# Performance work log

Hardware: AMD Instinct MI355X
Metric: run time of the kernel (lower is better)

The kernel has to match this reference:

```python
import jax, jax.numpy as jnp
import numpy as np

F = 1024      # features
CF = 768      # context_features
H = 8         # num_heads
D = 64        # head_features
MID = H * D   # 512
SCALE = D ** -0.5


def _ln(x, g, b):
    m = jnp.mean(x, axis=-1, keepdims=True)
    v = jnp.var(x, axis=-1, keepdims=True)
    return (x - m) / jnp.sqrt(v + 1e-5) * g + b


def _attention(x, ctx, ng, nb, ncg, ncb, wq, wkv, wo, bo):
    # pre-norms (Attention.forward)
    xn = _ln(x, ng, nb)
    cn = _ln(ctx, ncg, ncb)
    q = xn @ wq                              # [b, n, MID]
    k, v = jnp.split(cn @ wkv, 2, axis=-1)   # [b, m, MID] each
    b, n, _ = q.shape
    m = k.shape[1]
    q = q.reshape(b, n, H, D).transpose(0, 2, 1, 3)  # b h n d
    k = k.reshape(b, m, H, D).transpose(0, 2, 1, 3)
    v = v.reshape(b, m, H, D).transpose(0, 2, 1, 3)
    sim = jnp.einsum('bhnd,bhmd->bhnm', q, k) * SCALE   # use_rel_pos=False
    attn = jax.nn.softmax(sim, axis=-1)
    out = jnp.einsum('bhnm,bhmd->bhnd', attn, v)
    out = out.transpose(0, 2, 1, 3).reshape(b, n, MID)
    return out @ wo + bo


def setup_inputs() -> dict:
    key = jax.random.key(0)
    ks = jax.random.split(key, 16)
    s = 0.02
    inp = {
        'x': jax.random.normal(ks[0], (4, 2048, F), jnp.float32),
        'context': jax.random.normal(ks[1], (4, 512, CF), jnp.float32),
        # self-attention params
        'sa_ng': jnp.ones((F,), jnp.float32),
        'sa_nb': jnp.zeros((F,), jnp.float32),
        'sa_ncg': jnp.ones((F,), jnp.float32),
        'sa_ncb': jnp.zeros((F,), jnp.float32),
        'sa_wq': jax.random.normal(ks[2], (F, MID), jnp.float32) * s,
        'sa_wkv': jax.random.normal(ks[3], (F, 2 * MID), jnp.float32) * s,
        'sa_wo': jax.random.normal(ks[4], (MID, F), jnp.float32) * s,
        'sa_bo': jnp.zeros((F,), jnp.float32),
        # cross-attention params
        'ca_ng': jnp.ones((F,), jnp.float32),
        'ca_nb': jnp.zeros((F,), jnp.float32),
        'ca_ncg': jnp.ones((CF,), jnp.float32),
        'ca_ncb': jnp.zeros((CF,), jnp.float32),
        'ca_wq': jax.random.normal(ks[5], (F, MID), jnp.float32) * s,
        'ca_wkv': jax.random.normal(ks[6], (CF, 2 * MID), jnp.float32) * s,
        'ca_wo': jax.random.normal(ks[7], (MID, F), jnp.float32) * s,
        'ca_bo': jnp.zeros((F,), jnp.float32),
    }
    return inp


def reference(x, context,
              sa_ng, sa_nb, sa_ncg, sa_ncb, sa_wq, sa_wkv, sa_wo, sa_bo,
              ca_ng, ca_nb, ca_ncg, ca_ncb, ca_wq, ca_wkv, ca_wo, ca_bo):
    # AttentionBlock.forward: x = self_attn(x) + x; x = cross_attn(x, ctx) + x
    x = _attention(x, x, sa_ng, sa_nb, sa_ncg, sa_ncb, sa_wq, sa_wkv, sa_wo, sa_bo) + x
    x = _attention(x, context, ca_ng, ca_nb, ca_ncg, ca_ncb, ca_wq, ca_wkv, ca_wo, ca_bo) + x
    return x
```

## Files before the change

### kernel.cpp

```cpp
#include <hip/hip_runtime.h>
#include <hip/hip_bf16.h>

typedef __bf16 bf16x8 __attribute__((ext_vector_type(8)));
typedef float  f32x4  __attribute__((ext_vector_type(4)));

#define MFMA16(a, b, c) __builtin_amdgcn_mfma_f32_16x16x32_bf16((a), (b), (c), 0, 0, 0)

__device__ __forceinline__ float fast_exp2(float x) {
#if __has_builtin(__builtin_amdgcn_exp2f)
    return __builtin_amdgcn_exp2f(x);
#else
    return exp2f(x);
#endif
}

__device__ __forceinline__ void async16(void* lds, const void* g) {
    __builtin_amdgcn_global_load_lds(
        (const __attribute__((address_space(1))) unsigned int*)g,
        (__attribute__((address_space(3))) unsigned int*)lds, 16, 0, 0);
}

__device__ __forceinline__ void tconv_tile(const float* __restrict__ W,
                                           __bf16* __restrict__ WT,
                                           int K, int N, int id, int nbx,
                                           __bf16 (*t)[65]) {
    int n0 = (id % nbx) * 64, k0 = (id / nbx) * 64;
    int tx = threadIdx.x & 63, ty = threadIdx.x >> 6;
#pragma unroll
    for (int r = ty; r < 64; r += 4)
        t[r][tx] = (__bf16)W[(size_t)(k0 + r) * N + n0 + tx];
    __syncthreads();
#pragma unroll
    for (int rr = ty; rr < 64; rr += 4)
        WT[(size_t)(n0 + rr) * K + k0 + tx] = t[tx][rr];
}

__global__ __launch_bounds__(256) void tconv6_kernel(
    const float* W0, __bf16* T0, const float* W1, __bf16* T1,
    const float* W2, __bf16* T2, const float* W3, __bf16* T3,
    const float* W4, __bf16* T4, const float* W5, __bf16* T5) {
    __shared__ __bf16 t[64][65];
    int id = blockIdx.x;
    if (id < 128)      tconv_tile(W0, T0, 1024, 512,  id,       8,  t);
    else if (id < 384) tconv_tile(W1, T1, 1024, 1024, id - 128, 16, t);
    else if (id < 512) tconv_tile(W2, T2, 512,  1024, id - 384, 16, t);
    else if (id < 640) tconv_tile(W3, T3, 1024, 512,  id - 512, 8,  t);
    else if (id < 832) tconv_tile(W4, T4, 768,  1024, id - 640, 16, t);
    else               tconv_tile(W5, T5, 512,  1024, id - 832, 16, t);
}

template <int C>
__device__ __forceinline__ void ln_body(const float* __restrict__ xr,
                                        const float* __restrict__ g,
                                        const float* __restrict__ b,
                                        __bf16* __restrict__ orow,
                                        float* p1, float* p2) {
    constexpr int NP = (C == 1024) ? 4 : 3;
    float v[NP], s1 = 0.f, s2 = 0.f;
    if constexpr (C == 1024) {
        float4 f = *(const float4*)&xr[threadIdx.x * 4];
        v[0] = f.x; v[1] = f.y; v[2] = f.z; v[3] = f.w;
#pragma unroll
        for (int i = 0; i < 4; i++) { s1 += v[i]; s2 += v[i] * v[i]; }
    } else {
#pragma unroll
        for (int i = 0; i < 3; i++) {
            v[i] = xr[threadIdx.x + i * 256];
            s1 += v[i]; s2 += v[i] * v[i];
        }
    }
#pragma unroll
    for (int off = 1; off < 64; off <<= 1) {
        s1 += __shfl_xor(s1, off);
        s2 += __shfl_xor(s2, off);
    }
    int wave = threadIdx.x >> 6;
    if ((threadIdx.x & 63) == 0) { p1[wave] = s1; p2[wave] = s2; }
    __syncthreads();
    s1 = p1[0] + p1[1] + p1[2] + p1[3];
    s2 = p2[0] + p2[1] + p2[2] + p2[3];
    float mean = s1 / C;
    float rstd = rsqrtf(s2 / C - mean * mean + 1e-5f);
    if constexpr (C == 1024) {
        union { __bf16 h[4]; unsigned long long u; } pk;
#pragma unroll
        for (int i = 0; i < 4; i++) {
            int c = threadIdx.x * 4 + i;
            pk.h[i] = (__bf16)((v[i] - mean) * rstd * g[c] + b[c]);
        }
        *(unsigned long long*)&orow[threadIdx.x * 4] = pk.u;
    } else {
#pragma unroll
        for (int i = 0; i < 3; i++) {
            int c = threadIdx.x + i * 256;
            orow[c] = (__bf16)((v[i] - mean) * rstd * g[c] + b[c]);
        }
    }
}

__global__ __launch_bounds__(256) void ln2_kernel(const float* __restrict__ x,
                                                  const float* __restrict__ g1,
                                                  const float* __restrict__ b1,
                                                  const float* __restrict__ g2,
                                                  const float* __restrict__ b2,
                                                  __bf16* __restrict__ o1,
                                                  __bf16* __restrict__ o2) {
    constexpr int C = 1024;
    int row = blockIdx.x;
    const float* xr = x + (size_t)row * C;
    float4 f = *(const float4*)&xr[threadIdx.x * 4];
    float v[4] = {f.x, f.y, f.z, f.w};
    float s1 = 0.f, s2 = 0.f;
#pragma unroll
    for (int i = 0; i < 4; i++) { s1 += v[i]; s2 += v[i] * v[i]; }
#pragma unroll
    for (int off = 1; off < 64; off <<= 1) {
        s1 += __shfl_xor(s1, off);
        s2 += __shfl_xor(s2, off);
    }
    __shared__ float p1[4], p2[4];
    int wave = threadIdx.x >> 6;
    if ((threadIdx.x & 63) == 0) { p1[wave] = s1; p2[wave] = s2; }
    __syncthreads();
    s1 = p1[0] + p1[1] + p1[2] + p1[3];
    s2 = p2[0] + p2[1] + p2[2] + p2[3];
    float mean = s1 / C;
    float rstd = rsqrtf(s2 / C - mean * mean + 1e-5f);
    union { __bf16 h[4]; unsigned long long u; } pk1, pk2;
#pragma unroll
    for (int i = 0; i < 4; i++) {
        int c = threadIdx.x * 4 + i;
        float nv = (v[i] - mean) * rstd;
        pk1.h[i] = (__bf16)(nv * g1[c] + b1[c]);
        pk2.h[i] = (__bf16)(nv * g2[c] + b2[c]);
    }
    *(unsigned long long*)&o1[(size_t)row * C + threadIdx.x * 4] = pk1.u;
    *(unsigned long long*)&o2[(size_t)row * C + threadIdx.x * 4] = pk2.u;
}

__global__ __launch_bounds__(256) void ln_cross_kernel(
    const float* __restrict__ x1, const float* __restrict__ g1, const float* __restrict__ b1,
    __bf16* __restrict__ o1,
    const float* __restrict__ ctx, const float* __restrict__ g2, const float* __restrict__ b2,
    __bf16* __restrict__ o2, int rows1) {
    __shared__ float p1[4], p2[4];
    int id = blockIdx.x;
    if (id < rows1) {
        ln_body<1024>(x1 + (size_t)id * 1024, g1, b1, o1 + (size_t)id * 1024, p1, p2);
    } else {
        int row = id - rows1;
        ln_body<768>(ctx + (size_t)row * 768, g2, b2, o2 + (size_t)row * 768, p1, p2);
    }
}

template <int EPI>
__device__ __forceinline__ void gemm_core(const __bf16* __restrict__ A,
                                          const __bf16* __restrict__ BT,
                                          void* __restrict__ Cout,
                                          int N, int K, int bm, int bn,
                                          const float* __restrict__ bias,
                                          const float* __restrict__ res,
                                          float scale,
                                          __bf16* Al, __bf16* Bl) {
    int tid = threadIdx.x;
    int lane = tid & 63, wave = tid >> 6;
    int quad = lane >> 4, l15 = lane & 15;
    int wm = wave >> 1, wn = wave & 1;
    const __bf16* Ab = A + (size_t)(bm * 128) * K;
    const __bf16* Bb = BT + (size_t)(bn * 128) * K;
    f32x4 acc[4][4] = {};
    for (int k0 = 0; k0 < K; k0 += 64) {
#pragma unroll
        for (int j = 0; j < 4; j++) {
            int sbase = wave * 256 + j * 64;
            int s = sbase + lane;
            int r = s >> 3, c = (s & 7) ^ (r & 7);
            async16((char*)Al + sbase * 16, &Ab[(size_t)r * K + k0 + c * 8]);
            async16((char*)Bl + sbase * 16, &Bb[(size_t)r * K + k0 + c * 8]);
        }
        __syncthreads();
#pragma unroll
        for (int ks = 0; ks < 2; ks++) {
            bf16x8 a[4], b[4];
#pragma unroll
            for (int i = 0; i < 4; i++) {
                int row = wm * 64 + i * 16 + l15;
                a[i] = *(const bf16x8*)&Al[row * 64 + ((ks * 4 + quad) ^ (row & 7)) * 8];
            }
#pragma unroll
            for (int t = 0; t < 4; t++) {
                int row = wn * 64 + t * 16 + l15;
                b[t] = *(const bf16x8*)&Bl[row * 64 + ((ks * 4 + quad) ^ (row & 7)) * 8];
            }
#pragma unroll
            for (int i = 0; i < 4; i++)
#pragma unroll
                for (int t = 0; t < 4; t++) acc[i][t] = MFMA16(a[i], b[t], acc[i][t]);
        }
        __syncthreads();
    }
#pragma unroll
    for (int i = 0; i < 4; i++) {
#pragma unroll
        for (int t = 0; t < 4; t++) {
#pragma unroll
            for (int r = 0; r < 4; r++) {
                int row = bm * 128 + wm * 64 + i * 16 + quad * 4 + r;
                int col = bn * 128 + wn * 64 + t * 16 + l15;
                float vv = acc[i][t][r];
                if (EPI == 0) {
                    ((__bf16*)Cout)[(size_t)row * N + col] = (__bf16)(vv * scale);
                } else {
                    ((float*)Cout)[(size_t)row * N + col] =
                        vv + bias[col] + res[(size_t)row * N + col];
                }
            }
        }
    }
}

template <int EPI>
__global__ __launch_bounds__(256) void gemm_bt(const __bf16* __restrict__ A,
                                               const __bf16* __restrict__ BT,
                                               void* __restrict__ Cout,
                                               int M, int N, int K,
                                               const float* __restrict__ bias,
                                               const float* __restrict__ res) {
    __shared__ __align__(16) __bf16 Al[128 * 64];
    __shared__ __align__(16) __bf16 Bl[128 * 64];
    gemm_core<EPI>(A, BT, Cout, N, K, blockIdx.x, blockIdx.y, bias, res, 1.0f, Al, Bl);
}

__global__ __launch_bounds__(256) void gemm_fused3(
    const __bf16* A0, const __bf16* B0, __bf16* C0, int N0, int K0, int nbn0, float sc0,
    const __bf16* A1, const __bf16* B1, __bf16* C1, int N1, int K1, int nbn1, float sc1,
    const __bf16* A2, const __bf16* B2, __bf16* C2, int N2, int K2, int nbn2, float sc2,
    int c0, int c1) {
    __shared__ __align__(16) __bf16 Al[128 * 64];
    __shared__ __align__(16) __bf16 Bl[128 * 64];
    int id = blockIdx.x;
    if (id < c0) {
        gemm_core<0>(A0, B0, C0, N0, K0, id / nbn0, id % nbn0, nullptr, nullptr, sc0, Al, Bl);
    } else if (id < c1) {
        id -= c0;
        gemm_core<0>(A1, B1, C1, N1, K1, id / nbn1, id % nbn1, nullptr, nullptr, sc1, Al, Bl);
    } else {
        id -= c1;
        gemm_core<0>(A2, B2, C2, N2, K2, id / nbn2, id % nbn2, nullptr, nullptr, sc2, Al, Bl);
    }
}

__global__ __launch_bounds__(256) void flash_kernel(const __bf16* __restrict__ q,
                                                    const __bf16* __restrict__ kb,
                                                    const __bf16* __restrict__ vt,
                                                    __bf16* __restrict__ out,
                                                    int n, int m) {
    __shared__ __align__(16) __bf16 Qs[64 * 64];
    __shared__ __align__(16) __bf16 Ks[64 * 64];
    __shared__ __align__(16) __bf16 VTs[64 * 64];
    __shared__ __align__(16) __bf16 Ps[64 * 64];
    int tid = threadIdx.x;
    int lane = tid & 63, w = tid >> 6;
    int quad = lane >> 4, l15 = lane & 15;
    int qt = blockIdx.x, h = blockIdx.y, b = blockIdx.z;
    const size_t BM = (size_t)gridDim.z * m;
    const int qrow = w * 16 + l15;

#pragma unroll
    for (int j = 0; j < 2; j++) {
        int sbase = w * 128 + j * 64;
        int s = sbase + lane;
        int r = s >> 3, c = (s & 7) ^ (r & 7);
        async16((char*)Qs + sbase * 16,
                &q[(size_t)(b * n + qt * 64 + r) * 512 + h * 64 + c * 8]);
    }

    f32x4 acc[4] = {};
    float l_part = 0.f;

    int nkt = m / 64;
    for (int kt = 0; kt < nkt; kt++) {
#pragma unroll
        for (int j = 0; j < 2; j++) {
            int sbase = w * 128 + j * 64;
            int s = sbase + lane;
            int r = s >> 3, c = (s & 7) ^ (r & 7);
            async16((char*)Ks + sbase * 16,
                    &kb[(size_t)(b * m + kt * 64 + r) * 512 + h * 64 + c * 8]);
            async16((char*)VTs + sbase * 16,
                    &vt[(size_t)(h * 64 + r) * BM + b * m + kt * 64 + c * 8]);
        }
        __syncthreads();

        f32x4 sacc[4] = {};
#pragma unroll
        for (int kk = 0; kk < 64; kk += 32) {
            int jb = ((kk >> 3) + quad) ^ (qrow & 7);
            bf16x8 bq = *(const bf16x8*)&Qs[qrow * 64 + jb * 8];
#pragma unroll
            for (int t = 0; t < 4; t++) {
                int krow = t * 16 + l15;
                int ja = ((kk >> 3) + quad) ^ (krow & 7);
                bf16x8 ak = *(const bf16x8*)&Ks[krow * 64 + ja * 8];
                sacc[t] = MFMA16(ak, bq, sacc[t]);
            }
        }

#pragma unroll
        for (int t = 0; t < 4; t++) {
            float e0 = fast_exp2(sacc[t][0]);
            float e1 = fast_exp2(sacc[t][1]);
            float e2 = fast_exp2(sacc[t][2]);
            float e3 = fast_exp2(sacc[t][3]);
            l_part += (e0 + e1) + (e2 + e3);
            union { __bf16 h[4]; unsigned long long u; } pk;
            pk.h[0] = (__bf16)e0; pk.h[1] = (__bf16)e1;
            pk.h[2] = (__bf16)e2; pk.h[3] = (__bf16)e3;
            int chunk = t * 2 + (quad >> 1);
            int off = qrow * 64 + (chunk ^ (qrow & 7)) * 8 + (quad & 1) * 4;
            *(unsigned long long*)&Ps[off] = pk.u;
        }

#pragma unroll
        for (int kk = 0; kk < 64; kk += 32) {
            int jp = ((kk >> 3) + quad) ^ (qrow & 7);
            bf16x8 ap = *(const bf16x8*)&Ps[qrow * 64 + jp * 8];
#pragma unroll
            for (int t2 = 0; t2 < 4; t2++) {
                int drow = t2 * 16 + l15;
                int jv = ((kk >> 3) + quad) ^ (drow & 7);
                bf16x8 bv = *(const bf16x8*)&VTs[drow * 64 + jv * 8];
                acc[t2] = MFMA16(ap, bv, acc[t2]);
            }
        }
        __syncthreads();
    }

    l_part += __shfl_xor(l_part, 16);
    l_part += __shfl_xor(l_part, 32);
    float rinv = 1.0f / l_part;
#pragma unroll
    for (int r = 0; r < 4; r++) {
        float rl = __shfl(rinv, quad * 4 + r);
        int row = b * n + qt * 64 + w * 16 + quad * 4 + r;
#pragma unroll
        for (int t2 = 0; t2 < 4; t2++)
            out[(size_t)row * 512 + h * 64 + t2 * 16 + l15] =
                (__bf16)(acc[t2][r] * rl);
    }
}

extern "C" void kernel_launch(void* const* d_in, const int* in_sizes, int n_in,
                              void* d_out, int out_size, void* d_ws, size_t ws_size,
                              hipStream_t stream) {
    const float* x      = (const float*)d_in[0];
    const float* ctx    = (const float*)d_in[1];
    const float* sa_ng  = (const float*)d_in[2];
    const float* sa_nb  = (const float*)d_in[3];
    const float* sa_ncg = (const float*)d_in[4];
    const float* sa_ncb = (const float*)d_in[5];
    const float* sa_wq  = (const float*)d_in[6];
    const float* sa_wkv = (const float*)d_in[7];
    const float* sa_wo  = (const float*)d_in[8];
    const float* sa_bo  = (const float*)d_in[9];
    const float* ca_ng  = (const float*)d_in[10];
    const float* ca_nb  = (const float*)d_in[11];
    const float* ca_ncg = (const float*)d_in[12];
    const float* ca_ncb = (const float*)d_in[13];
    const float* ca_wq  = (const float*)d_in[14];
    const float* ca_wkv = (const float*)d_in[15];
    const float* ca_wo  = (const float*)d_in[16];
    const float* ca_bo  = (const float*)d_in[17];
    float* out = (float*)d_out;

    const int B = 4, N = 2048, M = 512, F = 1024, CF = 768, MID = 512;
    const int ROWS = B * N;
    const int CROWS = B * M;
    const float QSCALE = 0.125f * 1.4426950408889634f;

    char* ws = (char*)d_ws;
    size_t off = 0;
    auto alloc = [&](size_t bytes) {
        void* p = ws + off;
        off = (off + bytes + 255) & ~(size_t)255;
        return p;
    };
    __bf16* wqT   = (__bf16*)alloc((size_t)MID * F * 2);
    __bf16* wkvT  = (__bf16*)alloc((size_t)(2 * MID) * F * 2);
    __bf16* woT   = (__bf16*)alloc((size_t)F * MID * 2);
    __bf16* cwqT  = (__bf16*)alloc((size_t)MID * F * 2);
    __bf16* cwkvT = (__bf16*)alloc((size_t)(2 * MID) * CF * 2);
    __bf16* cwoT  = (__bf16*)alloc((size_t)F * MID * 2);
    __bf16* xn1   = (__bf16*)alloc((size_t)ROWS * F * 2);
    __bf16* xn2   = (__bf16*)alloc((size_t)ROWS * F * 2);
    __bf16* qb    = (__bf16*)alloc((size_t)ROWS * MID * 2);
    __bf16* kb    = (__bf16*)alloc((size_t)ROWS * MID * 2);
    __bf16* vt    = (__bf16*)alloc((size_t)MID * ROWS * 2);
    __bf16* ao    = (__bf16*)alloc((size_t)ROWS * MID * 2);
    float*  x1    = (float*)alloc((size_t)ROWS * F * 4);
    (void)ws_size; (void)in_sizes; (void)n_in; (void)out_size;

    dim3 blk(256);

    tconv6_kernel<<<dim3(960), blk, 0, stream>>>(
        sa_wq, wqT, sa_wkv, wkvT, sa_wo, woT, ca_wq, cwqT, ca_wkv, cwkvT, ca_wo, cwoT);

    ln2_kernel<<<dim3(ROWS), blk, 0, stream>>>(x, sa_ng, sa_nb, sa_ncg, sa_ncb, xn1, xn2);
    {
        int c0 = (ROWS / 128) * (MID / 128);
        int c1 = c0 + (ROWS / 128) * (MID / 128);
        int c2 = c1 + (MID / 128) * (ROWS / 128);
        gemm_fused3<<<dim3(c2), blk, 0, stream>>>(
            xn1, wqT, qb, MID, F, MID / 128, QSCALE,
            xn2, wkvT, kb, MID, F, MID / 128, 1.0f,
            wkvT + (size_t)MID * F, xn2, vt, ROWS, F, ROWS / 128, 1.0f,
            c0, c1);
    }
    flash_kernel<<<dim3(N / 64, 8, B), blk, 0, stream>>>(qb, kb, vt, ao, N, N);
    gemm_bt<1><<<dim3(ROWS / 128, F / 128), blk, 0, stream>>>(
        ao, woT, x1, ROWS, F, MID, sa_bo, x);

    ln_cross_kernel<<<dim3(ROWS + CROWS), blk, 0, stream>>>(
        x1, ca_ng, ca_nb, xn1, ctx, ca_ncg, ca_ncb, xn2, ROWS);
    {
        int c0 = (ROWS / 128) * (MID / 128);
        int c1 = c0 + (CROWS / 128) * (MID / 128);
        int c2 = c1 + (MID / 128) * (CROWS / 128);
        gemm_fused3<<<dim3(c2), blk, 0, stream>>>(
            xn1, cwqT, qb, MID, F, MID / 128, QSCALE,
            xn2, cwkvT, kb, MID, CF, MID / 128, 1.0f,
            cwkvT + (size_t)MID * CF, xn2, vt, CROWS, CF, CROWS / 128, 1.0f,
            c0, c1);
    }
    flash_kernel<<<dim3(N / 64, 8, B), blk, 0, stream>>>(qb, kb, vt, ao, N, M);
    gemm_bt<1><<<dim3(ROWS / 128, F / 128), blk, 0, stream>>>(
        ao, cwoT, out, ROWS, F, MID, ca_bo, x1);
}
```

Baseline: 325.8 us.

## Double-buffer K/V tiles in flash kernel and keep Q in registers

```diff
diff --git a/kernel.cpp b/kernel.cpp
--- a/kernel.cpp
+++ b/kernel.cpp
@@ -255,9 +255,8 @@
                                                     const __bf16* __restrict__ vt,
                                                     __bf16* __restrict__ out,
                                                     int n, int m) {
-    __shared__ __align__(16) __bf16 Qs[64 * 64];
-    __shared__ __align__(16) __bf16 Ks[64 * 64];
-    __shared__ __align__(16) __bf16 VTs[64 * 64];
+    __shared__ __align__(16) __bf16 Ks[2][64 * 64];
+    __shared__ __align__(16) __bf16 VTs[2][64 * 64];
     __shared__ __align__(16) __bf16 Ps[64 * 64];
     int tid = threadIdx.x;
     int lane = tid & 63, w = tid >> 6;
@@ -266,42 +265,53 @@
     const size_t BM = (size_t)gridDim.z * m;
     const int qrow = w * 16 + l15;
 
-#pragma unroll
-    for (int j = 0; j < 2; j++) {
-        int sbase = w * 128 + j * 64;
-        int s = sbase + lane;
-        int r = s >> 3, c = (s & 7) ^ (r & 7);
-        async16((char*)Qs + sbase * 16,
-                &q[(size_t)(b * n + qt * 64 + r) * 512 + h * 64 + c * 8]);
-    }
+    const __bf16* qrp = &q[(size_t)(b * n + qt * 64 + qrow) * 512 + h * 64];
+    bf16x8 bq0 = *(const bf16x8*)&qrp[quad * 8];
+    bf16x8 bq1 = *(const bf16x8*)&qrp[(4 + quad) * 8];
+
+    int s0 = w * 128 + lane, s1 = s0 + 64;
+    int r0 = s0 >> 3, c0 = (s0 & 7) ^ (r0 & 7);
+    int r1 = s1 >> 3, c1 = (s1 & 7) ^ (r1 & 7);
+    const int sb0 = (w * 128) * 16, sb1 = sb0 + 64 * 16;
+    const __bf16* ksrc0 = &kb[(size_t)(b * m + r0) * 512 + h * 64 + (size_t)c0 * 8];
+    const __bf16* ksrc1 = &kb[(size_t)(b * m + r1) * 512 + h * 64 + (size_t)c1 * 8];
+    const __bf16* vsrc0 = &vt[(size_t)(h * 64 + r0) * BM + b * m + (size_t)c0 * 8];
+    const __bf16* vsrc1 = &vt[(size_t)(h * 64 + r1) * BM + b * m + (size_t)c1 * 8];
+    const size_t kadv = (size_t)64 * 512;
+    const int vadv = 64;
 
     f32x4 acc[4] = {};
     float l_part = 0.f;
-
     int nkt = m / 64;
+
+    async16((char*)Ks[0] + sb0, ksrc0);
+    async16((char*)Ks[0] + sb1, ksrc1);
+    async16((char*)VTs[0] + sb0, vsrc0);
+    async16((char*)VTs[0] + sb1, vsrc1);
+
     for (int kt = 0; kt < nkt; kt++) {
-#pragma unroll
-        for (int j = 0; j < 2; j++) {
-            int sbase = w * 128 + j * 64;
-            int s = sbase + lane;
-            int r = s >> 3, c = (s & 7) ^ (r & 7);
-            async16((char*)Ks + sbase * 16,
-                    &kb[(size_t)(b * m + kt * 64 + r) * 512 + h * 64 + c * 8]);
-            async16((char*)VTs + sbase * 16,
-                    &vt[(size_t)(h * 64 + r) * BM + b * m + kt * 64 + c * 8]);
-        }
+        const __bf16* Kc = Ks[kt & 1];
+        const __bf16* Vc = VTs[kt & 1];
         __syncthreads();
+        if (kt + 1 < nkt) {
+            __bf16* Kn = Ks[(kt + 1) & 1];
+            __bf16* Vn = VTs[(kt + 1) & 1];
+            ksrc0 += kadv; ksrc1 += kadv; vsrc0 += vadv; vsrc1 += vadv;
+            async16((char*)Kn + sb0, ksrc0);
+            async16((char*)Kn + sb1, ksrc1);
+            async16((char*)Vn + sb0, vsrc0);
+            async16((char*)Vn + sb1, vsrc1);
+        }
 
         f32x4 sacc[4] = {};
 #pragma unroll
         for (int kk = 0; kk < 64; kk += 32) {
-            int jb = ((kk >> 3) + quad) ^ (qrow & 7);
-            bf16x8 bq = *(const bf16x8*)&Qs[qrow * 64 + jb * 8];
+            bf16x8 bq = (kk == 0) ? bq0 : bq1;
 #pragma unroll
             for (int t = 0; t < 4; t++) {
                 int krow = t * 16 + l15;
                 int ja = ((kk >> 3) + quad) ^ (krow & 7);
-                bf16x8 ak = *(const bf16x8*)&Ks[krow * 64 + ja * 8];
+                bf16x8 ak = *(const bf16x8*)&Kc[krow * 64 + ja * 8];
                 sacc[t] = MFMA16(ak, bq, sacc[t]);
             }
         }
@@ -329,11 +339,10 @@
             for (int t2 = 0; t2 < 4; t2++) {
                 int drow = t2 * 16 + l15;
                 int jv = ((kk >> 3) + quad) ^ (drow & 7);
-                bf16x8 bv = *(const bf16x8*)&VTs[drow * 64 + jv * 8];
+                bf16x8 bv = *(const bf16x8*)&Vc[drow * 64 + jv * 8];
                 acc[t2] = MFMA16(ap, bv, acc[t2]);
             }
         }
-        __syncthreads();
     }
 
     l_part += __shfl_xor(l_part, 16);
```

New measurement: 318.7 us. 1.02x faster.

## Split flash attention KV tiles across waves with register-resident fragments and LDS reduction

Applied to the files above, without the earlier changes.

```diff
diff --git a/kernel.cpp b/kernel.cpp
--- a/kernel.cpp
+++ b/kernel.cpp
@@ -250,103 +250,155 @@
     }
 }
 
-__global__ __launch_bounds__(256) void flash_kernel(const __bf16* __restrict__ q,
-                                                    const __bf16* __restrict__ kb,
-                                                    const __bf16* __restrict__ vt,
-                                                    __bf16* __restrict__ out,
-                                                    int n, int m) {
-    __shared__ __align__(16) __bf16 Qs[64 * 64];
-    __shared__ __align__(16) __bf16 Ks[64 * 64];
-    __shared__ __align__(16) __bf16 VTs[64 * 64];
-    __shared__ __align__(16) __bf16 Ps[64 * 64];
+__global__ __launch_bounds__(256, 2) void flash_kernel(const __bf16* __restrict__ q,
+                                                       const __bf16* __restrict__ kb,
+                                                       const __bf16* __restrict__ vt,
+                                                       __bf16* __restrict__ out,
+                                                       int n, int m) {
+    __shared__ __align__(16) __bf16 Ps[4][64 * 64];
+    __shared__ float Lred[4][64];
     int tid = threadIdx.x;
     int lane = tid & 63, w = tid >> 6;
     int quad = lane >> 4, l15 = lane & 15;
     int qt = blockIdx.x, h = blockIdx.y, b = blockIdx.z;
     const size_t BM = (size_t)gridDim.z * m;
-    const int qrow = w * 16 + l15;
-
-#pragma unroll
-    for (int j = 0; j < 2; j++) {
-        int sbase = w * 128 + j * 64;
-        int s = sbase + lane;
-        int r = s >> 3, c = (s & 7) ^ (r & 7);
-        async16((char*)Qs + sbase * 16,
-                &q[(size_t)(b * n + qt * 64 + r) * 512 + h * 64 + c * 8]);
-    }
-
-    f32x4 acc[4] = {};
-    float l_part = 0.f;
+
+    const __bf16* qbase = q + (size_t)(b * n + qt * 64) * 512 + h * 64;
+    bf16x8 qf[2][4];
+#pragma unroll
+    for (int s = 0; s < 2; s++)
+#pragma unroll
+        for (int u = 0; u < 4; u++)
+            qf[s][u] = *(const bf16x8*)&qbase[(u * 16 + l15) * 512 + s * 32 + quad * 8];
+
+    const __bf16* kbase = kb + (size_t)(b * m) * 512 + h * 64;
+    const __bf16* vbase = vt + (size_t)(h * 64) * BM + b * m;
+
+    auto kaddr = [&](int kt, int s, int t) {
+        return &kbase[(size_t)(kt * 64 + t * 16 + l15) * 512 + s * 32 + quad * 8];
+    };
+    auto vaddr = [&](int kt, int s, int t2) {
+        return &vbase[(size_t)(t2 * 16 + l15) * BM + kt * 64 + s * 32 + quad * 8];
+    };
 
     int nkt = m / 64;
-    for (int kt = 0; kt < nkt; kt++) {
-#pragma unroll
-        for (int j = 0; j < 2; j++) {
-            int sbase = w * 128 + j * 64;
-            int s = sbase + lane;
-            int r = s >> 3, c = (s & 7) ^ (r & 7);
-            async16((char*)Ks + sbase * 16,
-                    &kb[(size_t)(b * m + kt * 64 + r) * 512 + h * 64 + c * 8]);
-            async16((char*)VTs + sbase * 16,
-                    &vt[(size_t)(h * 64 + r) * BM + b * m + kt * 64 + c * 8]);
-        }
+    int niter = nkt / 4;
+    int kt0 = w;
+
+    bf16x8 kf[2][4], vf[2][4];
+#pragma unroll
+    for (int s = 0; s < 2; s++)
+#pragma unroll
+        for (int t = 0; t < 4; t++) {
+            kf[s][t] = *(const bf16x8*)kaddr(kt0, s, t);
+            vf[s][t] = *(const bf16x8*)vaddr(kt0, s, t);
+        }
+
+    f32x4 acc[4][4] = {};
+    float lp[4] = {0.f, 0.f, 0.f, 0.f};
+    __bf16* Pw = Ps[w];
+
+    for (int i = 0; i < niter; i++) {
+        int ktn = kt0 + (i + 1) * 4;
+        bool hasnext = (i + 1 < niter);
+
+#pragma unroll
+        for (int t = 0; t < 4; t++) {
+            f32x4 sacc[4] = {};
+#pragma unroll
+            for (int s = 0; s < 2; s++)
+#pragma unroll
+                for (int u = 0; u < 4; u++)
+                    sacc[u] = MFMA16(kf[s][t], qf[s][u], sacc[u]);
+#pragma unroll
+            for (int u = 0; u < 4; u++) {
+                float e0 = fast_exp2(sacc[u][0]);
+                float e1 = fast_exp2(sacc[u][1]);
+                float e2 = fast_exp2(sacc[u][2]);
+                float e3 = fast_exp2(sacc[u][3]);
+                lp[u] += (e0 + e1) + (e2 + e3);
+                union { __bf16 h[4]; unsigned long long uu; } pk;
+                pk.h[0] = (__bf16)e0; pk.h[1] = (__bf16)e1;
+                pk.h[2] = (__bf16)e2; pk.h[3] = (__bf16)e3;
+                int qp = u * 16 + l15;
+                int chunk = t * 2 + (quad >> 1);
+                int off = qp * 64 + (chunk ^ (qp & 7)) * 8 + (quad & 1) * 4;
+                *(unsigned long long*)&Pw[off] = pk.uu;
+            }
+        }
+
+        if (hasnext) {
+#pragma unroll
+            for (int s = 0; s < 2; s++)
+#pragma unroll
+                for (int t = 0; t < 4; t++)
+                    kf[s][t] = *(const bf16x8*)kaddr(ktn, s, t);
+        }
+
+#pragma unroll
+        for (int s = 0; s < 2; s++) {
+            bf16x8 ap[4];
+#pragma unroll
+            for (int u = 0; u < 4; u++) {
+                int qp = u * 16 + l15;
+                ap[u] = *(const bf16x8*)&Pw[qp * 64 + ((s * 4 + quad) ^ (qp & 7)) * 8];
+            }
+#pragma unroll
+            for (int t2 = 0; t2 < 4; t2++)
+#pragma unroll
+                for (int u = 0; u < 4; u++)
+                    acc[u][t2] = MFMA16(ap[u], vf[s][t2], acc[u][t2]);
+        }
+
+        if (hasnext) {
+#pragma unroll
+            for (int s = 0; s < 2; s++)
+#pragma unroll
+                for (int t = 0; t < 4; t++)
+                    vf[s][t] = *(const bf16x8*)vaddr(ktn, s, t);
+        }
+    }
+
+#pragma unroll
+    for (int u = 0; u < 4; u++) {
+        lp[u] += __shfl_xor(lp[u], 16);
+        lp[u] += __shfl_xor(lp[u], 32);
+    }
+    if (quad == 0) {
+#pragma unroll
+        for (int u = 0; u < 4; u++) Lred[w][u * 16 + l15] = lp[u];
+    }
+    __syncthreads();
+    int qq = w * 16 + (lane >> 2);
+    int dbase = (lane & 3) * 8;
+    float lt = Lred[0][qq] + Lred[1][qq] + Lred[2][qq] + Lred[3][qq];
+    float rq = 1.0f / lt;
+    float* Fbuf = (float*)&Ps[0][0];
+#pragma unroll
+    for (int half = 0; half < 2; half++) {
         __syncthreads();
-
-        f32x4 sacc[4] = {};
-#pragma unroll
-        for (int kk = 0; kk < 64; kk += 32) {
-            int jb = ((kk >> 3) + quad) ^ (qrow & 7);
-            bf16x8 bq = *(const bf16x8*)&Qs[qrow * 64 + jb * 8];
-#pragma unroll
-            for (int t = 0; t < 4; t++) {
-                int krow = t * 16 + l15;
-                int ja = ((kk >> 3) + quad) ^ (krow & 7);
-                bf16x8 ak = *(const bf16x8*)&Ks[krow * 64 + ja * 8];
-                sacc[t] = MFMA16(ak, bq, sacc[t]);
-            }
-        }
-
-#pragma unroll
-        for (int t = 0; t < 4; t++) {
-            float e0 = fast_exp2(sacc[t][0]);
-            float e1 = fast_exp2(sacc[t][1]);
-            float e2 = fast_exp2(sacc[t][2]);
-            float e3 = fast_exp2(sacc[t][3]);
-            l_part += (e0 + e1) + (e2 + e3);
-            union { __bf16 h[4]; unsigned long long u; } pk;
-            pk.h[0] = (__bf16)e0; pk.h[1] = (__bf16)e1;
-            pk.h[2] = (__bf16)e2; pk.h[3] = (__bf16)e3;
-            int chunk = t * 2 + (quad >> 1);
-            int off = qrow * 64 + (chunk ^ (qrow & 7)) * 8 + (quad & 1) * 4;
-            *(unsigned long long*)&Ps[off] = pk.u;
-        }
-
-#pragma unroll
-        for (int kk = 0; kk < 64; kk += 32) {
-            int jp = ((kk >> 3) + quad) ^ (qrow & 7);
-            bf16x8 ap = *(const bf16x8*)&Ps[qrow * 64 + jp * 8];
-#pragma unroll
-            for (int t2 = 0; t2 < 4; t2++) {
-                int drow = t2 * 16 + l15;
-                int jv = ((kk >> 3) + quad) ^ (drow & 7);
-                bf16x8 bv = *(const bf16x8*)&VTs[drow * 64 + jv * 8];
-                acc[t2] = MFMA16(ap, bv, acc[t2]);
-            }
-        }
+#pragma unroll
+        for (int u = 0; u < 4; u++)
+#pragma unroll
+            for (int tt = 0; tt < 2; tt++)
+#pragma unroll
+                for (int r = 0; r < 4; r++) {
+                    int qrow2 = u * 16 + quad * 4 + r;
+                    Fbuf[w * 2048 + qrow2 * 32 + tt * 16 + l15] = acc[u][half * 2 + tt][r];
+                }
         __syncthreads();
-    }
-
-    l_part += __shfl_xor(l_part, 16);
-    l_part += __shfl_xor(l_part, 32);
-    float rinv = 1.0f / l_part;
-#pragma unroll
-    for (int r = 0; r < 4; r++) {
-        float rl = __shfl(rinv, quad * 4 + r);
-        int row = b * n + qt * 64 + w * 16 + quad * 4 + r;
-#pragma unroll
-        for (int t2 = 0; t2 < 4; t2++)
-            out[(size_t)row * 512 + h * 64 + t2 * 16 + l15] =
-                (__bf16)(acc[t2][r] * rl);
+        float o[8] = {};
+#pragma unroll
+        for (int wv = 0; wv < 4; wv++) {
+            const float4* sp = (const float4*)&Fbuf[wv * 2048 + qq * 32 + dbase];
+            float4 a = sp[0], c = sp[1];
+            o[0] += a.x; o[1] += a.y; o[2] += a.z; o[3] += a.w;
+            o[4] += c.x; o[5] += c.y; o[6] += c.z; o[7] += c.w;
+        }
+        union { __bf16 h[8]; bf16x8 v; } pk8;
+#pragma unroll
+        for (int j = 0; j < 8; j++) pk8.h[j] = (__bf16)(o[j] * rq);
+        *(bf16x8*)&out[(size_t)(b * n + qt * 64 + qq) * 512 + h * 64 + half * 32 + dbase] = pk8.v;
     }
 }
 
```

Measured after the change: 379.1 us. 16.4% more time.
